# Kernel tuning notes

Hardware: AMD Instinct MI355X
Metric: run time of the kernel (lower is better)

Reference implementation:

```python
import jax, jax.numpy as jnp
import numpy as np

N, E, F_IN, H, D = 50000, 800000, 128, 4, 32
NEG_SLOPE = 0.2

def setup_inputs() -> dict:
    key = jax.random.key(0)
    ks = jax.random.split(key, 8)
    x = jax.random.normal(ks[0], (N, F_IN), dtype=jnp.float32)
    src = jax.random.randint(ks[1], (E,), 0, N, dtype=jnp.int32)
    dst = jax.random.randint(ks[2], (E,), 0, N, dtype=jnp.int32)
    s = 1.0 / np.sqrt(F_IN)
    W_src = jax.random.uniform(ks[3], (F_IN, H * D), jnp.float32, -s, s)
    b_src = jnp.zeros((H * D,), jnp.float32)
    W_dst = jax.random.uniform(ks[4], (F_IN, H * D), jnp.float32, -s, s)
    b_dst = jnp.zeros((H * D,), jnp.float32)
    attn = jax.random.normal(ks[5], (H, D), dtype=jnp.float32) / np.sqrt(D)
    return {"x": x, "src": src, "dst": dst, "W_src": W_src, "b_src": b_src,
            "W_dst": W_dst, "b_dst": b_dst, "attn": attn}

def reference(x, src, dst, W_src, b_src, W_dst, b_dst, attn):
    n = x.shape[0]
    # dense projections: [N, H, D]
    fs = (x @ W_src + b_src).reshape(n, H, D)
    fd = (x @ W_dst + b_dst).reshape(n, H, D)
    # GATv2 edge score: a^T leaky_relu(W_l x_u + W_r x_v)
    e = jax.nn.leaky_relu(fs[src] + fd[dst], NEG_SLOPE)  # [E, H, D]
    score = jnp.einsum('ehd,hd->eh', e, attn)            # [E, H]
    # segment softmax over incoming edges of each dst node
    smax = jax.ops.segment_max(score, dst, num_segments=n)
    smax = jnp.where(jnp.isfinite(smax), smax, 0.0)
    ex = jnp.exp(score - smax[dst])
    denom = jax.ops.segment_sum(ex, dst, num_segments=n)
    alpha = ex / denom[dst]                              # [E, H]
    # scatter-weighted aggregation of src features
    h = jax.ops.segment_sum(alpha[:, :, None] * fs[src], dst, num_segments=n)
    h = jax.nn.relu(h)                                   # activation=relu
    return h.reshape(n, H * D)
```

## Files before the change

kernel.cpp:

```cpp
#include <hip/hip_runtime.h>
#include <hip/hip_fp16.h>

#define NN 50000
#define NE 800000
#define FIN 128
#define NH 4
#define HD 32
#define FOUT 128
#define NEG 0.2f
#define NB_W    ((256 * FIN + 255) / 256)
#define N_GEMM  782
#define NBKT    98
#define CHUNK   4096
#define NCHUNK  ((NE + CHUNK - 1) / CHUNK)
#define GB_GRID 980
#define BCAP    12288

typedef __attribute__((ext_vector_type(8))) short bf16x8;
typedef __attribute__((ext_vector_type(4))) float f32x4;

__device__ __forceinline__ uint f2bf_u(float f) {
    uint u = __float_as_uint(f);
    u += 0x7FFF + ((u >> 16) & 1);
    return u >> 16;
}
__device__ __forceinline__ ushort f2bf(float f) { return (ushort)f2bf_u(f); }

template<int CTRL>
__device__ __forceinline__ float dpp_add(float x) {
    int y = __builtin_amdgcn_update_dpp(0, __float_as_int(x), CTRL, 0xF, 0xF, false);
    return x + __int_as_float(y);
}
#define DPP_QUAD_XOR1 0xB1
#define DPP_QUAD_XOR2 0x4E

__device__ __forceinline__ __half2 u2h(uint u) { return __builtin_bit_cast(__half2, u); }
__device__ __forceinline__ uint h2u(__half2 h) { return __builtin_bit_cast(uint, h); }

__device__ __forceinline__ __half2 hmax2(__half2 a, __half2 b) {
    uint r, ua = h2u(a), ub = h2u(b);
    asm("v_pk_max_f16 %0, %1, %2" : "=v"(r) : "v"(ua), "v"(ub));
    return u2h(r);
}

__global__ __launch_bounds__(256) void hist_wt_k(
    const int* __restrict__ dst, int* __restrict__ chunk_hist,
    const float* __restrict__ Wsrc, const float* __restrict__ Wdst,
    ushort* __restrict__ Wt,
    const float* __restrict__ attn, __half* __restrict__ attn_h)
{
    __shared__ int hist[NBKT];
    const int b = blockIdx.x;
    const int tid = threadIdx.x;
    if (b < NCHUNK) {
        const int e0 = b * CHUNK;
        for (int t = tid; t < NBKT; t += 256) hist[t] = 0;
        __syncthreads();
        #pragma unroll
        for (int k = 0; k < 16; ++k) {
            const int e = e0 + k * 256 + tid;
            if (e < NE) atomicAdd(&hist[dst[e] >> 9], 1);
        }
        __syncthreads();
        for (int t = tid; t < NBKT; t += 256)
            chunk_hist[b * NBKT + t] = hist[t];
    } else {
        if (b == NCHUNK && tid < FOUT) attn_h[tid] = __float2half(attn[tid]);
        int t = (b - NCHUNK) * 256 + tid;
        if (t >= 256 * FIN) return;
        int n = t >> 7, k = t & 127;
        float v = (n < 128) ? Wsrc[k * 128 + n] : Wdst[k * 128 + (n - 128)];
        Wt[t] = f2bf(v);
    }
}

__global__ __launch_bounds__(256) void gemm_scatter_k(
    const float* __restrict__ x, const ushort* __restrict__ Wt,
    const float* __restrict__ bsrc, const float* __restrict__ bdst,
    __half* __restrict__ fsfd,
    const int* __restrict__ dst, const int* __restrict__ src,
    const int* __restrict__ chunk_hist, int* __restrict__ bkbase,
    uint* __restrict__ ebuf)
{
    __shared__ ushort As[64 * 128];
    __shared__ ushort Bs[64 * 128];
    __shared__ int cur[NBKT];
    __shared__ int ps[256];
    const int b = blockIdx.x;
    const int tid = threadIdx.x;

    if (b % 5 == 0) {
        const int chunk = b / 5;
        int total = 0, part = 0;
        if (tid < NBKT) {
            for (int c = 0; c < NCHUNK; ++c) {
                const int h = chunk_hist[c * NBKT + tid];
                total += h;
                part += (c < chunk) ? h : 0;
            }
        }
        ps[tid] = (tid < NBKT) ? total : 0;
        __syncthreads();
        for (int off = 1; off < 256; off <<= 1) {
            int add = (tid >= off) ? ps[tid - off] : 0;
            __syncthreads();
            ps[tid] += add;
            __syncthreads();
        }
        if (tid < NBKT) cur[tid] = (ps[tid] - total) + part;
        if (chunk == 0) {
            if (tid < NBKT) bkbase[tid] = ps[tid] - total;
            if (tid == 0) bkbase[NBKT] = NE;
        }
        __syncthreads();
        const int e0 = chunk * CHUNK;
        #pragma unroll
        for (int k = 0; k < 16; ++k) {
            const int e = e0 + k * 256 + tid;
            if (e < NE) {
                const int d = dst[e];
                const int p = atomicAdd(&cur[d >> 9], 1);
                ebuf[p] = ((uint)d << 16) | (uint)src[e];
            }
        }
        return;
    }

    const int g = b - b / 5 - 1;
    if (g >= N_GEMM) return;
    const int bm = g * 64;

    for (int q = tid; q < 64 * 16; q += 256) {
        int r = q >> 4, c16 = q & 15;
        int row = bm + r;
        uint4 o = make_uint4(0u, 0u, 0u, 0u);
        if (row < NN) {
            const float4 a = *(const float4*)&x[(size_t)row * FIN + c16 * 8];
            const float4 c = *(const float4*)&x[(size_t)row * FIN + c16 * 8 + 4];
            o.x = f2bf_u(a.x) | (f2bf_u(a.y) << 16);
            o.y = f2bf_u(a.z) | (f2bf_u(a.w) << 16);
            o.z = f2bf_u(c.x) | (f2bf_u(c.y) << 16);
            o.w = f2bf_u(c.z) | (f2bf_u(c.w) << 16);
        }
        int off = r * 256 + ((c16 * 16) ^ ((r & 7) << 4));
        *(uint4*)((char*)As + off) = o;
    }

    const int wid = tid >> 6, lane = tid & 63;
    const int wr = (wid >> 1) * 32, wc = (wid & 1) * 32;
    const int lrow = lane & 15;
    const int lk = (lane >> 4) * 16;

    #pragma unroll
    for (int ct = 0; ct < 4; ++ct) {
        if (ct > 0) __syncthreads();
        for (int q = tid; q < 64 * 16; q += 256) {
            int r = q >> 4, c16 = q & 15;
            uint4 v = *(const uint4*)&Wt[(ct * 64 + r) * FIN + c16 * 8];
            int off = r * 256 + ((c16 * 16) ^ ((r & 7) << 4));
            *(uint4*)((char*)Bs + off) = v;
        }
        __syncthreads();

        f32x4 acc[2][2] = {};
        #pragma unroll
        for (int kk = 0; kk < 4; ++kk) {
            bf16x8 a[2], bb[2];
            #pragma unroll
            for (int m = 0; m < 2; ++m) {
                int r = wr + m * 16 + lrow;
                int off = r * 256 + ((kk * 64 + lk) ^ ((r & 7) << 4));
                a[m] = *(bf16x8*)((char*)As + off);
            }
            #pragma unroll
            for (int n = 0; n < 2; ++n) {
                int r = wc + n * 16 + lrow;
                int off = r * 256 + ((kk * 64 + lk) ^ ((r & 7) << 4));
                bb[n] = *(bf16x8*)((char*)Bs + off);
            }
            #pragma unroll
            for (int m = 0; m < 2; ++m)
                #pragma unroll
                for (int n = 0; n < 2; ++n)
                    acc[m][n] = __builtin_amdgcn_mfma_f32_16x16x32_bf16(a[m], bb[n], acc[m][n], 0, 0, 0);
        }

        #pragma unroll
        for (int m = 0; m < 2; ++m) {
            #pragma unroll
            for (int n = 0; n < 2; ++n) {
                int gcol = ct * 64 + wc + n * 16 + (lane & 15);
                float bias = (gcol < 128) ? bsrc[gcol] : bdst[gcol - 128];
                #pragma unroll
                for (int r = 0; r < 4; ++r) {
                    int grow = bm + wr + m * 16 + (lane >> 4) * 4 + r;
                    if (grow < NN)
                        fsfd[(size_t)grow * 256 + gcol] = __float2half(acc[m][n][r] + bias);
                }
            }
        }
    }
}

__global__ __launch_bounds__(256) void binB_k(
    const uint* __restrict__ ebuf, const int* __restrict__ bkbase,
    int* __restrict__ rowptr, ushort* __restrict__ nbr)
{
    __shared__ int cnt_s[512];
    __shared__ int ps[256];
    __shared__ ushort buf[BCAP];
    const int b = blockIdx.x;
    const int tid = threadIdx.x;
    const int node0 = b << 9;
    const int nodes = (node0 + 512 < NN) ? 512 : (NN - node0);
    const int segbase = bkbase[b];
    const int segend  = bkbase[b + 1];
    const int seglen  = segend - segbase;

    cnt_s[tid] = 0;
    cnt_s[tid + 256] = 0;
    __syncthreads();
    for (int i = segbase + tid; i < segend; i += 256)
        atomicAdd(&cnt_s[(int)(ebuf[i] >> 16) - node0], 1);
    __syncthreads();

    const int c0 = cnt_s[2 * tid], c1 = cnt_s[2 * tid + 1];
    const int pair = c0 + c1;
    ps[tid] = pair;
    __syncthreads();
    for (int off = 1; off < 256; off <<= 1) {
        int add = (tid >= off) ? ps[tid - off] : 0;
        __syncthreads();
        ps[tid] += add;
        __syncthreads();
    }
    const int ex = ps[tid] - pair;
    __syncthreads();
    cnt_s[2 * tid] = ex;
    cnt_s[2 * tid + 1] = ex + c0;
    if (2 * tid < nodes)     rowptr[node0 + 2 * tid]     = segbase + ex;
    if (2 * tid + 1 < nodes) rowptr[node0 + 2 * tid + 1] = segbase + ex + c0;
    if (b == NBKT - 1 && tid == 0) rowptr[NN] = segend;
    __syncthreads();

    if (seglen <= BCAP) {
        for (int i = segbase + tid; i < segend; i += 256) {
            const uint e = ebuf[i];
            const int d = (int)(e >> 16) - node0;
            const int p = atomicAdd(&cnt_s[d], 1);
            buf[p] = (ushort)(e & 0xffffu);
        }
        __syncthreads();
        for (int i = tid; i < seglen; i += 256)
            nbr[segbase + i] = buf[i];
    } else {
        for (int i = segbase + tid; i < segend; i += 256) {
            const uint e = ebuf[i];
            const int d = (int)(e >> 16) - node0;
            const int p = atomicAdd(&cnt_s[d], 1);
            nbr[segbase + p] = (ushort)(e & 0xffffu);
        }
    }
}

__global__ __launch_bounds__(256) void gat_node_k(
    const __half* __restrict__ fsfd, const __half* __restrict__ attn_h,
    const int* __restrict__ rowptr, const ushort* __restrict__ nbr,
    float* __restrict__ out)
{
    const int node = blockIdx.x * 4 + (threadIdx.x >> 6);
    const int lane = threadIdx.x & 63;
    const int ql = lane & 15;
    const int q  = lane >> 4;

    const uint4 ufd = *(const uint4*)&fsfd[(size_t)node * 256 + 128 + 8 * ql];
    const __half2 fd0 = u2h(ufd.x), fd1 = u2h(ufd.y), fd2 = u2h(ufd.z), fd3 = u2h(ufd.w);
    const uint4 uav = *(const uint4*)&attn_h[8 * ql];
    const __half2 av0 = u2h(uav.x), av1 = u2h(uav.y), av2 = u2h(uav.z), av3 = u2h(uav.w);
    const __half2 k02 = __float2half2_rn(NEG);

    const int beg = rowptr[node];
    const int end = rowptr[node + 1];

    float den = 0.f;
    __half2 acc0 = u2h(0), acc1 = u2h(0), acc2 = u2h(0), acc3 = u2h(0);

    for (int i = beg; i < end; i += 16) {
        #pragma unroll
        for (int j = 0; j < 4; ++j) {
            const int idx = i + 4 * j + q;
            const bool valid = idx < end;
            const int s = nbr[valid ? idx : end - 1];
            const uint4 u = *(const uint4*)&fsfd[(size_t)s * 256 + 8 * ql];
            const __half2 f0 = u2h(u.x), f1 = u2h(u.y), f2 = u2h(u.z), f3 = u2h(u.w);
            __half2 v0 = __hadd2(f0, fd0), v1 = __hadd2(f1, fd1);
            __half2 v2 = __hadd2(f2, fd2), v3 = __hadd2(f3, fd3);
            v0 = hmax2(v0, __hmul2(v0, k02));
            v1 = hmax2(v1, __hmul2(v1, k02));
            v2 = hmax2(v2, __hmul2(v2, k02));
            v3 = hmax2(v3, __hmul2(v3, k02));
            __half2 sch = __hmul2(v0, av0);
            sch = __hfma2(v1, av1, sch);
            sch = __hfma2(v2, av2, sch);
            sch = __hfma2(v3, av3, sch);
            float sc = __low2float(sch) + __high2float(sch);
            sc = dpp_add<DPP_QUAD_XOR1>(sc);
            sc = dpp_add<DPP_QUAD_XOR2>(sc);
            float ex = __expf(sc);
            ex = valid ? ex : 0.f;
            den += ex;
            const __half2 exh = __float2half2_rn(ex);
            acc0 = __hfma2(exh, f0, acc0);
            acc1 = __hfma2(exh, f1, acc1);
            acc2 = __hfma2(exh, f2, acc2);
            acc3 = __hfma2(exh, f3, acc3);
        }
    }

    den += __shfl_xor(den, 16, 64);
    den += __shfl_xor(den, 32, 64);
    uint ua0 = h2u(acc0), ua1 = h2u(acc1), ua2 = h2u(acc2), ua3 = h2u(acc3);
    ua0 = h2u(__hadd2(u2h(ua0), u2h((uint)__shfl_xor((int)ua0, 16, 64))));
    ua1 = h2u(__hadd2(u2h(ua1), u2h((uint)__shfl_xor((int)ua1, 16, 64))));
    ua2 = h2u(__hadd2(u2h(ua2), u2h((uint)__shfl_xor((int)ua2, 16, 64))));
    ua3 = h2u(__hadd2(u2h(ua3), u2h((uint)__shfl_xor((int)ua3, 16, 64))));
    ua0 = h2u(__hadd2(u2h(ua0), u2h((uint)__shfl_xor((int)ua0, 32, 64))));
    ua1 = h2u(__hadd2(u2h(ua1), u2h((uint)__shfl_xor((int)ua1, 32, 64))));
    ua2 = h2u(__hadd2(u2h(ua2), u2h((uint)__shfl_xor((int)ua2, 32, 64))));
    ua3 = h2u(__hadd2(u2h(ua3), u2h((uint)__shfl_xor((int)ua3, 32, 64))));

    if (q == 0) {
        const float inv = (den > 0.f) ? 1.f / den : 0.f;
        float4 o0, o1;
        o0.x = fmaxf(__low2float(u2h(ua0))  * inv, 0.f);
        o0.y = fmaxf(__high2float(u2h(ua0)) * inv, 0.f);
        o0.z = fmaxf(__low2float(u2h(ua1))  * inv, 0.f);
        o0.w = fmaxf(__high2float(u2h(ua1)) * inv, 0.f);
        o1.x = fmaxf(__low2float(u2h(ua2))  * inv, 0.f);
        o1.y = fmaxf(__high2float(u2h(ua2)) * inv, 0.f);
        o1.z = fmaxf(__low2float(u2h(ua3))  * inv, 0.f);
        o1.w = fmaxf(__high2float(u2h(ua3)) * inv, 0.f);
        *(float4*)&out[(size_t)node * FOUT + 8 * ql] = o0;
        *(float4*)&out[(size_t)node * FOUT + 8 * ql + 4] = o1;
    }
}

extern "C" void kernel_launch(void* const* d_in, const int* in_sizes, int n_in,
                              void* d_out, int out_size, void* d_ws, size_t ws_size,
                              hipStream_t stream)
{
    const float* x    = (const float*)d_in[0];
    const int*   src  = (const int*)d_in[1];
    const int*   dst  = (const int*)d_in[2];
    const float* Wsrc = (const float*)d_in[3];
    const float* bsrc = (const float*)d_in[4];
    const float* Wdst = (const float*)d_in[5];
    const float* bdst = (const float*)d_in[6];
    const float* attn = (const float*)d_in[7];
    float* out = (float*)d_out;

    ushort* Wt      = (ushort*)d_ws;
    __half* fsfd    = (__half*)(Wt + 256 * FIN);
    int* chunk_hist = (int*)(fsfd + (size_t)NN * 256);
    int* bkbase     = chunk_hist + NCHUNK * NBKT;
    int* rowptr     = bkbase + NBKT + 1;
    uint* ebuf      = (uint*)(rowptr + NN + 1);
    ushort* nbr     = (ushort*)(ebuf + NE);
    __half* attn_h  = (__half*)(nbr + NE);

    hist_wt_k<<<NCHUNK + NB_W, 256, 0, stream>>>(dst, chunk_hist, Wsrc, Wdst, Wt, attn, attn_h);
    gemm_scatter_k<<<GB_GRID, 256, 0, stream>>>(x, Wt, bsrc, bdst, fsfd,
                                                dst, src, chunk_hist, bkbase, ebuf);
    binB_k<<<NBKT, 256, 0, stream>>>(ebuf, bkbase, rowptr, nbr);
    gat_node_k<<<(NN + 3) / 4, 256, 0, stream>>>(fsfd, attn_h, rowptr, nbr, out);
}
```

Measured before the change: 88.96 us.

## Load GEMM weights directly from global and transpose MFMA for vectorized stores

Drops the shared-memory staging of the weight tile, along with its per-column-tile barriers, and has each lane read its bf16x8 B fragment straight from global memory (the weights are small and likely cache-resident). It also swaps the MFMA operand order so each lane's accumulator holds four consecutive output columns of one row. That allows a float4 bias load and a packed 8-byte half store in place of four scalar strided stores. The cost is uncoalesced per-lane global loads of weights inside the inner loop, which relies on L1/L2 hits.

Measured after the change: 92.45 us. 1.04x slower.

```diff
diff --git a/kernel.cpp b/kernel.cpp
--- a/kernel.cpp
+++ b/kernel.cpp
@@ -25,6 +25,9 @@
     return u >> 16;
 }
 __device__ __forceinline__ ushort f2bf(float f) { return (ushort)f2bf_u(f); }
+__device__ __forceinline__ uint f2h_u(float f) {
+    return (uint)__builtin_bit_cast(ushort, __float2half(f));
+}
 
 template<int CTRL>
 __device__ __forceinline__ float dpp_add(float x) {
@@ -83,7 +86,6 @@
     uint* __restrict__ ebuf)
 {
     __shared__ ushort As[64 * 128];
-    __shared__ ushort Bs[64 * 128];
     __shared__ int cur[NBKT];
     __shared__ int ps[256];
     const int b = blockIdx.x;
@@ -145,23 +147,16 @@
         int off = r * 256 + ((c16 * 16) ^ ((r & 7) << 4));
         *(uint4*)((char*)As + off) = o;
     }
+    __syncthreads();
 
     const int wid = tid >> 6, lane = tid & 63;
     const int wr = (wid >> 1) * 32, wc = (wid & 1) * 32;
     const int lrow = lane & 15;
     const int lk = (lane >> 4) * 16;
+    const int kel = (lane >> 4) * 8;
 
     #pragma unroll
     for (int ct = 0; ct < 4; ++ct) {
-        if (ct > 0) __syncthreads();
-        for (int q = tid; q < 64 * 16; q += 256) {
-            int r = q >> 4, c16 = q & 15;
-            uint4 v = *(const uint4*)&Wt[(ct * 64 + r) * FIN + c16 * 8];
-            int off = r * 256 + ((c16 * 16) ^ ((r & 7) << 4));
-            *(uint4*)((char*)Bs + off) = v;
-        }
-        __syncthreads();
-
         f32x4 acc[2][2] = {};
         #pragma unroll
         for (int kk = 0; kk < 4; ++kk) {
@@ -174,29 +169,27 @@
             }
             #pragma unroll
             for (int n = 0; n < 2; ++n) {
-                int r = wc + n * 16 + lrow;
-                int off = r * 256 + ((kk * 64 + lk) ^ ((r & 7) << 4));
-                bb[n] = *(bf16x8*)((char*)Bs + off);
+                bb[n] = *(const bf16x8*)&Wt[(ct * 64 + wc + n * 16 + lrow) * FIN + kk * 32 + kel];
             }
             #pragma unroll
             for (int m = 0; m < 2; ++m)
                 #pragma unroll
                 for (int n = 0; n < 2; ++n)
-                    acc[m][n] = __builtin_amdgcn_mfma_f32_16x16x32_bf16(a[m], bb[n], acc[m][n], 0, 0, 0);
+                    acc[m][n] = __builtin_amdgcn_mfma_f32_16x16x32_bf16(bb[n], a[m], acc[m][n], 0, 0, 0);
         }
 
         #pragma unroll
         for (int m = 0; m < 2; ++m) {
+            const int grow = bm + wr + m * 16 + (lane & 15);
+            if (grow >= NN) continue;
             #pragma unroll
             for (int n = 0; n < 2; ++n) {
-                int gcol = ct * 64 + wc + n * 16 + (lane & 15);
-                float bias = (gcol < 128) ? bsrc[gcol] : bdst[gcol - 128];
-                #pragma unroll
-                for (int r = 0; r < 4; ++r) {
-                    int grow = bm + wr + m * 16 + (lane >> 4) * 4 + r;
-                    if (grow < NN)
-                        fsfd[(size_t)grow * 256 + gcol] = __float2half(acc[m][n][r] + bias);
-                }
+                const int gcolb = ct * 64 + wc + n * 16 + (lane >> 4) * 4;
+                const float4 b4 = (gcolb < 128) ? *(const float4*)&bsrc[gcolb]
+                                                : *(const float4*)&bdst[gcolb - 128];
+                uint lo = f2h_u(acc[m][n][0] + b4.x) | (f2h_u(acc[m][n][1] + b4.y) << 16);
+                uint hi = f2h_u(acc[m][n][2] + b4.z) | (f2h_u(acc[m][n][3] + b4.w) << 16);
+                *(uint2*)&fsfd[(size_t)grow * 256 + gcolb] = make_uint2(lo, hi);
             }
         }
     }
```
